# Performance work log

Hardware: AMD Instinct MI355X
Metric: run time of the kernel (lower is better)

Reference implementation:

```python
import jax, jax.numpy as jnp
import numpy as np

# dims: B batch, L residues, CS=c_s, N_EXP mHC streams, H heads, CH c_hidden,
# PQK/PV qk/v points, CZ=c_p pair channels, RANK z-factor rank, CZQ=CZ//4
B, L, CS, N_EXP, H, CH, PQK, PV, CZ, RANK = 4, 1024, 384, 4, 8, 64, 4, 8, 128, 2
CZQ = CZ // 4
SINKHORN_ITERS = 20


def quat_to_rot(q):
    q = q / jnp.sqrt((q * q).sum(-1, keepdims=True) + 1e-8)
    w, x, y, z = q[..., 0], q[..., 1], q[..., 2], q[..., 3]
    R = jnp.stack([
        1 - 2 * (y * y + z * z), 2 * (x * y - w * z), 2 * (x * z + w * y),
        2 * (x * y + w * z), 1 - 2 * (x * x + z * z), 2 * (y * z - w * x),
        2 * (x * z - w * y), 2 * (y * z + w * x), 1 - 2 * (x * x + y * y)], axis=-1)
    return R.reshape(q.shape[:-1] + (3, 3))


def layer_norm(x, g, b, eps=1e-5):
    mu = x.mean(-1, keepdims=True)
    var = ((x - mu) ** 2).mean(-1, keepdims=True)
    return (x - mu) * jax.lax.rsqrt(var + eps) * g + b


def sinkhorn(logits):
    # project onto doubly-stochastic matrices (Birkhoff polytope), fixed iters
    M = jnp.exp(logits - logits.max(axis=(-2, -1), keepdims=True))
    for _ in range(SINKHORN_ITERS):
        M = M / (M.sum(-1, keepdims=True) + 1e-8)
        M = M / (M.sum(-2, keepdims=True) + 1e-8)
    return M


def _forward(s, z_factor_1, z_factor_2, quat_t, trans, mask, b_pre, b_post, b_res,
             W_pre, W_post, W_res, alpha, Wq, Wk, Wv, Wq_pts, Wk_pts, Wv_pts,
             Wz_q, Wz_k, head_w, Wo, bo, ln1_g, ln1_b, Wt1, bt1, Wt2, bt2,
             Wt3, bt3, lnt_g, lnt_b, Wbb, bbb):
    # --- mHC: expand_input (first layer replicates stream) + dynamic mappings ---
    s_exp = jnp.broadcast_to(s[:, :, None, :], (B, L, N_EXP, CS))
    h = s_exp.reshape(B, L, N_EXP * CS)
    hn = h * jax.lax.rsqrt((h * h).mean(-1, keepdims=True) + 1e-6)
    H_pre = jax.nn.softmax(b_pre + alpha * (hn @ W_pre), -1)        # [B,L,n]
    H_post = 2.0 * jax.nn.sigmoid(b_post + alpha * (hn @ W_post))   # [B,L,n]
    H_res = sinkhorn(b_res + alpha * (hn @ W_res).reshape(B, L, N_EXP, N_EXP))
    s_c = jnp.einsum('bln,blnc->blc', H_pre, s_exp)                 # contraction

    rot = quat_to_rot(quat_t)                                       # [B,L,3,3]

    # --- Flash-IPA (dense math-equivalent reference) ---
    q = (s_c @ Wq).reshape(B, L, H, CH)
    k = (s_c @ Wk).reshape(B, L, H, CH)
    v = (s_c @ Wv).reshape(B, L, H, CH)
    qp = (s_c @ Wq_pts).reshape(B, L, H, PQK, 3)
    kp = (s_c @ Wk_pts).reshape(B, L, H, PQK, 3)
    vp = (s_c @ Wv_pts).reshape(B, L, H, PV, 3)

    def to_global(p):
        return jnp.einsum('blij,blhpj->blhpi', rot, p) + trans[:, :, None, None, :]

    qp_g, kp_g, vp_g = to_global(qp), to_global(kp), to_global(vp)

    # low-rank factorized pair bias (z = outer product of per-residue factors)
    zq = jnp.einsum('blrz,zh->blrh', z_factor_1, Wz_q)
    zk = jnp.einsum('blrz,zh->blrh', z_factor_1, Wz_k)
    bias = jnp.einsum('birh,bjrh->bhij', zq, zk)

    qk = jnp.einsum('bihc,bjhc->bhij', q, k) / np.sqrt(CH)
    qn = (qp_g ** 2).sum((-2, -1)).transpose(0, 2, 1)               # [B,H,L]
    kn = (kp_g ** 2).sum((-2, -1)).transpose(0, 2, 1)
    pdot = jnp.einsum('bihpd,bjhpd->bhij', qp_g, kp_g)
    d2 = qn[:, :, :, None] + kn[:, :, None, :] - 2.0 * pdot         # sum_p ||qp_i - kp_j||^2
    gamma = jax.nn.softplus(head_w)
    wC = np.sqrt(2.0 / (9.0 * PQK))
    wL = np.sqrt(1.0 / 3.0)
    logits = wL * (qk + bias) - (wL * wC * 0.5) * gamma[None, :, None, None] * d2
    logits = jnp.where(mask[:, None, None, :] > 0, logits, -1e9)
    a = jax.nn.softmax(logits, -1)

    o = jnp.einsum('bhij,bjhc->bihc', a, v).reshape(B, L, H * CH)
    opt_g = jnp.einsum('bhij,bjhpd->bihpd', a, vp_g)
    diff = opt_g - trans[:, :, None, None, :]
    opt_l = jnp.einsum('blij,blhpi->blhpj', rot, diff)              # R^T (x - t)
    opt_norm = jnp.sqrt((opt_l ** 2).sum(-1) + 1e-8)
    opair = jnp.einsum('bhij,bjhrc->bihrc', a, z_factor_2).reshape(B, L, H * RANK * CZQ)
    feat = jnp.concatenate([o, opt_l.reshape(B, L, H * PV * 3),
                            opt_norm.reshape(B, L, H * PV), opair], -1)
    ipa_out = feat @ Wo + bo

    # residual + (dropout=identity at eval) + LN + transition (residual MLP) + LN
    s1 = layer_norm(s_c + ipa_out, ln1_g, ln1_b)
    t1 = jax.nn.relu(s1 @ Wt1 + bt1)
    t2 = jax.nn.relu(t1 @ Wt2 + bt2)
    s_ipa = layer_norm(s1 + (t2 @ Wt3 + bt3), lnt_g, lnt_b)

    # backbone update: quaternion (1,b,c,d) + translation, composed with frame
    upd = s_ipa @ Wbb + bbb                                         # [B,L,6]
    quat_u = jnp.concatenate([jnp.ones((B, L, 1), upd.dtype), upd[..., :3]], -1)
    R_u = quat_to_rot(quat_u)
    rot_new = jnp.einsum('blij,bljk->blik', rot, R_u)
    trans_new = jnp.einsum('blij,blj->bli', rot, upd[..., 3:]) + trans

    # mHC combine: H_res @ s  +  H_post^T * s_ipa (broadcast over streams)
    s_out = jnp.einsum('blmn,blnc->blmc', H_res, s_exp) + H_post[..., None] * s_ipa[:, :, None, :]
    return s_out, rot_new, trans_new


def setup_inputs() -> dict:
    key = jax.random.key(0)
    ks = jax.random.split(key, 24)

    def nrm(k, shape, scale=1.0):
        return jax.random.normal(k, shape, jnp.float32) * scale

    FEAT = H * CH + H * PV * 4 + H * RANK * CZQ  # 512 + 256 + 512 = 1280
    return dict(
        s=nrm(ks[0], (B, L, CS)),
        z_factor_1=nrm(ks[1], (B, L, RANK, CZ)),
        z_factor_2=nrm(ks[2], (B, L, H, RANK, CZQ)),
        quat_t=nrm(ks[3], (B, L, 4)),
        trans=nrm(ks[4], (B, L, 3)),
        mask=jnp.ones((B, L), jnp.float32),
        b_pre=nrm(ks[5], (N_EXP,), 0.02),
        b_post=nrm(ks[6], (N_EXP,), 0.02),
        b_res=nrm(ks[7], (N_EXP, N_EXP), 0.02),
        W_pre=nrm(ks[8], (N_EXP * CS, N_EXP), 0.02),
        W_post=nrm(ks[9], (N_EXP * CS, N_EXP), 0.02),
        W_res=nrm(ks[10], (N_EXP * CS, N_EXP * N_EXP), 0.02),
        alpha=jnp.float32(0.01),
        Wq=nrm(ks[11], (CS, H * CH), 0.02),
        Wk=nrm(ks[12], (CS, H * CH), 0.02),
        Wv=nrm(ks[13], (CS, H * CH), 0.02),
        Wq_pts=nrm(ks[14], (CS, H * PQK * 3), 0.02),
        Wk_pts=nrm(ks[15], (CS, H * PQK * 3), 0.02),
        Wv_pts=nrm(ks[16], (CS, H * PV * 3), 0.02),
        Wz_q=nrm(ks[17], (CZ, H), 0.02),
        Wz_k=nrm(ks[18], (CZ, H), 0.02),
        head_w=jnp.zeros((H,), jnp.float32),
        Wo=nrm(ks[19], (FEAT, CS), 0.02),
        bo=jnp.zeros((CS,), jnp.float32),
        ln1_g=jnp.ones((CS,), jnp.float32),
        ln1_b=jnp.zeros((CS,), jnp.float32),
        Wt1=nrm(ks[20], (CS, CS), 0.02),
        bt1=jnp.zeros((CS,), jnp.float32),
        Wt2=nrm(ks[21], (CS, CS), 0.02),
        bt2=jnp.zeros((CS,), jnp.float32),
        Wt3=nrm(ks[22], (CS, CS), 0.02),
        bt3=jnp.zeros((CS,), jnp.float32),
        lnt_g=jnp.ones((CS,), jnp.float32),
        lnt_b=jnp.zeros((CS,), jnp.float32),
        Wbb=nrm(ks[23], (CS, 6), 0.02),
        bbb=jnp.zeros((6,), jnp.float32),
    )


def reference(s, z_factor_1, z_factor_2, quat_t, trans, mask, b_pre, b_post, b_res,
              W_pre, W_post, W_res, alpha, Wq, Wk, Wv, Wq_pts, Wk_pts, Wv_pts,
              Wz_q, Wz_k, head_w, Wo, bo, ln1_g, ln1_b, Wt1, bt1, Wt2, bt2,
              Wt3, bt3, lnt_g, lnt_b, Wbb, bbb):
    return _forward(s, z_factor_1, z_factor_2, quat_t, trans, mask, b_pre, b_post,
                    b_res, W_pre, W_post, W_res, alpha, Wq, Wk, Wv, Wq_pts, Wk_pts,
                    Wv_pts, Wz_q, Wz_k, head_w, Wo, bo, ln1_g, ln1_b, Wt1, bt1,
                    Wt2, bt2, Wt3, bt3, lnt_g, lnt_b, Wbb, bbb)
```

## Files before the change

### kernel.cpp

```cpp
#include <hip/hip_runtime.h>
#include <hip/hip_bf16.h>

typedef __hip_bfloat16 bf16;
typedef float f4v __attribute__((ext_vector_type(4)));
typedef short s8v __attribute__((ext_vector_type(8)));

#define CSD    384
#define LL     1024
#define NH     8
#define BL     4096
#define NPROJ  1920
#define QDP    96
#define VDP    160
#define FEATD  1280

#define OFF_S      0
#define OFF_Z1     1572864
#define OFF_Z2     2621440
#define OFF_QUAT   4718592
#define OFF_TRANS  4734976
#define OFF_MASK   4747264
#define OFF_BPOST  4751360
#define OFF_BRES   4751376
#define OFF_WPOST  4751392
#define OFF_WRES   4757536
#define OFF_ALPHA  4782112
#define OFF_WQ     4782128
#define OFF_WK     4978736
#define OFF_WV     5175344
#define OFF_WQP    5371952
#define OFF_WKP    5408816
#define OFF_WVP    5445680
#define OFF_WZQ    5519408
#define OFF_WZK    5520432
#define OFF_HEADW  5521456
#define OFF_WO     5521472
#define OFF_BO     6012992
#define OFF_LN1G   6013376
#define OFF_LN1B   6013760
#define OFF_WT1    6014144
#define OFF_BT1    6161600
#define OFF_WT2    6161984
#define OFF_BT2    6309440
#define OFF_WT3    6309824
#define OFF_BT3    6457280
#define OFF_LNTG   6457664
#define OFF_LNTB   6458048
#define OFF_WBB    6458432
#define OFF_BBB    6460736
#define IN_END     6460752

#define WS_FLAG    6460752
#define WS_WPOSTR  6460768
#define WS_WRESR   6462304
#define WS_HPOST   6468448
#define WS_ROWSUM  6484832
#define WS_ROTB    6501216
#define WS_WCATT   6538080
#define WS_PROJ    7275360
#define WS_QB      15139680
#define WS_KB      16712544
#define WS_VT      18285408
#define WS_WOT     20906848
#define WS_WT1T    21152608
#define WS_WT2T    21226336
#define WS_WT3T    21300064
#define WS_VROW    21373792

#define OUT_ROT 6291456
#define OUT_TR  6328320

#define NSEG 34

struct P36 { const void* p[36]; };

__device__ __forceinline__ float b2f(bf16 x) { return __bfloat162float(x); }

__device__ __forceinline__ short f2bs(float x) {
  unsigned u = __float_as_uint(x);
  u += 0x7FFFu + ((u >> 16) & 1u);
  return (short)(u >> 16);
}

__device__ __forceinline__ int packbf(float lo, float hi) {
  return (int)(unsigned short)f2bs(lo) | ((int)f2bs(hi) << 16);
}

__device__ __forceinline__ float wredf(float v) {
#pragma unroll
  for (int o = 1; o < 64; o <<= 1) v += __shfl_xor(v, o, 64);
  return v;
}

__global__ void detect_k(const unsigned int* __restrict__ mask_raw, int* __restrict__ flag) {
  if (threadIdx.x == 0 && blockIdx.x == 0) flag[0] = (mask_raw[0] == 0x3F803F80u) ? 1 : 0;
}

__global__ __launch_bounds__(256) void cvtall_k(P36 ptrs, float* __restrict__ dst, const int* __restrict__ flagp) {
  const int i = blockIdx.x * 256 + threadIdx.x;
  if (i >= IN_END) return;
  const int flag = flagp[0];
  const int seg_src_t[NSEG] = {0,1,2,3,4,5,7,8,10,11,12,13,14,15,16,17,18,19,20,21,22,23,24,25,26,27,28,29,30,31,32,33,34,35};
  const int seg_dst_t[NSEG] = {OFF_S,OFF_Z1,OFF_Z2,OFF_QUAT,OFF_TRANS,OFF_MASK,OFF_BPOST,OFF_BRES,OFF_WPOST,OFF_WRES,
                               OFF_ALPHA,OFF_WQ,OFF_WK,OFF_WV,OFF_WQP,OFF_WKP,OFF_WVP,OFF_WZQ,OFF_WZK,OFF_HEADW,
                               OFF_WO,OFF_BO,OFF_LN1G,OFF_LN1B,OFF_WT1,OFF_BT1,OFF_WT2,OFF_BT2,OFF_WT3,OFF_BT3,
                               OFF_LNTG,OFF_LNTB,OFF_WBB,OFF_BBB};
  const int seg_cnt_t[NSEG] = {1572864,1048576,2097152,16384,12288,4096,4,16,6144,24576,
                               1,196608,196608,196608,36864,36864,73728,1024,1024,8,
                               491520,384,384,384,147456,384,147456,384,147456,384,
                               384,384,2304,6};
  int off = i, cnt = seg_cnt_t[0];
  const void* sp = ptrs.p[0];
#pragma unroll
  for (int k = 1; k < NSEG; k++) {
    if (i >= seg_dst_t[k]) { off = i - seg_dst_t[k]; cnt = seg_cnt_t[k]; sp = ptrs.p[seg_src_t[k]]; }
  }
  float v = 0.f;
  if (off < cnt) {
    v = flag ? b2f(((const bf16*)sp)[off]) : ((const float*)sp)[off];
  }
  dst[i] = v;
}

__global__ __launch_bounds__(256) void wcatT_k(const float* __restrict__ Wq, const float* __restrict__ Wk,
                                               const float* __restrict__ Wv, const float* __restrict__ Wqp,
                                               const float* __restrict__ Wkp, const float* __restrict__ Wvp,
                                               short* __restrict__ WcatT) {
  int i = blockIdx.x * 256 + threadIdx.x;
  if (i >= CSD * NPROJ) return;
  int k = i / NPROJ, c = i % NPROJ;
  float v;
  if (c < 512)       v = Wq[k * 512 + c];
  else if (c < 1024) v = Wk[k * 512 + c - 512];
  else if (c < 1536) v = Wv[k * 512 + c - 1024];
  else if (c < 1632) v = Wqp[k * 96 + c - 1536];
  else if (c < 1728) v = Wkp[k * 96 + c - 1632];
  else               v = Wvp[k * 192 + c - 1728];
  WcatT[c * CSD + k] = f2bs(v);
}

__global__ __launch_bounds__(256) void wT_k(const float* __restrict__ W, short* __restrict__ Wt, int K, int N) {
  int i = blockIdx.x * 256 + threadIdx.x;
  if (i >= K * N) return;
  int k = i / N, n = i % N;
  Wt[(size_t)n * K + k] = f2bs(W[i]);
}

__global__ __launch_bounds__(256) void wreduce_k(const float* __restrict__ Wpost, const float* __restrict__ Wres,
                                                 float* __restrict__ WpostR, float* __restrict__ WresR) {
  int i = blockIdx.x * 256 + threadIdx.x;
  if (i < CSD * 4) {
    int c = i >> 2, n = i & 3;
    float s = 0.f;
#pragma unroll
    for (int blk = 0; blk < 4; blk++) s += Wpost[(blk * CSD + c) * 4 + n];
    WpostR[i] = s;
  }
  if (i < CSD * 16) {
    int c = i >> 4, n = i & 15;
    float s = 0.f;
#pragma unroll
    for (int blk = 0; blk < 4; blk++) s += Wres[(blk * CSD + c) * 16 + n];
    WresR[i] = s;
  }
}

__global__ __launch_bounds__(64) void mhc_k(const float* __restrict__ sF, const float* __restrict__ quat,
                                            const float* __restrict__ bpost, const float* __restrict__ bres,
                                            const float* __restrict__ alpha_p, const float* __restrict__ WpostR,
                                            const float* __restrict__ WresR, float* __restrict__ hpost,
                                            float* __restrict__ rowsum, float* __restrict__ rotb) {
  const int bl = blockIdx.x, t = threadIdx.x;
  const float* sr = sF + (size_t)bl * CSD;
  float ssq = 0.f, dp[4] = {0.f, 0.f, 0.f, 0.f}, dr[16];
#pragma unroll
  for (int n = 0; n < 16; n++) dr[n] = 0.f;
#pragma unroll
  for (int e = 0; e < 6; e++) {
    const int c = t + e * 64;
    const float sv = sr[c];
    ssq = fmaf(sv, sv, ssq);
#pragma unroll
    for (int n = 0; n < 4; n++) dp[n] = fmaf(sv, WpostR[c * 4 + n], dp[n]);
#pragma unroll
    for (int n = 0; n < 16; n++) dr[n] = fmaf(sv, WresR[c * 16 + n], dr[n]);
  }
  ssq = wredf(ssq);
#pragma unroll
  for (int n = 0; n < 4; n++) dp[n] = wredf(dp[n]);
#pragma unroll
  for (int n = 0; n < 16; n++) dr[n] = wredf(dr[n]);
  const float alpha = alpha_p[0];
  const float invn = rsqrtf(ssq * (1.f / 384.f) + 1e-6f);
  if (t == 0) {
#pragma unroll
    for (int n = 0; n < 4; n++) {
      const float x = bpost[n] + alpha * invn * dp[n];
      hpost[bl * 4 + n] = 2.f / (1.f + __expf(-x));
    }
    float M[16];
    float mx = -1e30f;
#pragma unroll
    for (int k = 0; k < 16; k++) { M[k] = bres[k] + alpha * invn * dr[k]; mx = fmaxf(mx, M[k]); }
#pragma unroll
    for (int k = 0; k < 16; k++) M[k] = __expf(M[k] - mx);
    for (int it = 0; it < 20; it++) {
#pragma unroll
      for (int r = 0; r < 4; r++) {
        const float s4 = M[r * 4] + M[r * 4 + 1] + M[r * 4 + 2] + M[r * 4 + 3];
        const float iv = 1.f / (s4 + 1e-8f);
        M[r * 4] *= iv; M[r * 4 + 1] *= iv; M[r * 4 + 2] *= iv; M[r * 4 + 3] *= iv;
      }
#pragma unroll
      for (int c2 = 0; c2 < 4; c2++) {
        const float s4 = M[c2] + M[4 + c2] + M[8 + c2] + M[12 + c2];
        const float iv = 1.f / (s4 + 1e-8f);
        M[c2] *= iv; M[4 + c2] *= iv; M[8 + c2] *= iv; M[12 + c2] *= iv;
      }
    }
#pragma unroll
    for (int r = 0; r < 4; r++)
      rowsum[bl * 4 + r] = M[r * 4] + M[r * 4 + 1] + M[r * 4 + 2] + M[r * 4 + 3];
  }
  if (t == 1) {
    float w = quat[bl * 4 + 0], x = quat[bl * 4 + 1];
    float y = quat[bl * 4 + 2], z = quat[bl * 4 + 3];
    const float iq = rsqrtf(w * w + x * x + y * y + z * z + 1e-8f);
    w *= iq; x *= iq; y *= iq; z *= iq;
    float* R = rotb + (size_t)bl * 9;
    R[0] = 1.f - 2.f * (y * y + z * z); R[1] = 2.f * (x * y - w * z); R[2] = 2.f * (x * z + w * y);
    R[3] = 2.f * (x * y + w * z); R[4] = 1.f - 2.f * (x * x + z * z); R[5] = 2.f * (y * z - w * x);
    R[6] = 2.f * (x * z - w * y); R[7] = 2.f * (y * z + w * x); R[8] = 1.f - 2.f * (x * x + y * y);
  }
}

__global__ __launch_bounds__(256) void gemm_mfma_k(const float* __restrict__ A, const short* __restrict__ Bt,
                                                   const float* __restrict__ bias, float* __restrict__ C,
                                                   int M, int N, int K, int relu) {
  __shared__ __align__(16) short As[128 * 40];
  __shared__ __align__(16) short Bs[128 * 40];
  const int tid = threadIdx.x;
  const int wid = tid >> 6, lane = tid & 63;
  const int c15 = lane & 15, q = lane >> 4;
  const int bm = blockIdx.y, bn = blockIdx.x;
  const int m_wave = (wid & 1) * 64, n_wave = (wid >> 1) * 64;
  const float* Ab = A + (size_t)(bm * 128) * K;
  const short* Bb = Bt + (size_t)(bn * 128) * K;

  f4v acc[4][4];
#pragma unroll
  for (int mi = 0; mi < 4; mi++)
#pragma unroll
    for (int ni = 0; ni < 4; ni++) acc[mi][ni] = (f4v){0.f, 0.f, 0.f, 0.f};

  for (int k0 = 0; k0 < K; k0 += 32) {
    __syncthreads();
#pragma unroll
    for (int e = 0; e < 4; e++) {
      const int slot = tid + e * 256;
      const int m = slot >> 3, k4 = (slot & 7) * 4;
      const float4 a = *(const float4*)(Ab + (size_t)m * K + k0 + k4);
      short pk[4] = {f2bs(a.x), f2bs(a.y), f2bs(a.z), f2bs(a.w)};
      *(int2*)&As[m * 40 + k4] = *(const int2*)pk;
    }
#pragma unroll
    for (int e = 0; e < 2; e++) {
      const int slot = tid + e * 256;
      const int n = slot >> 2, k8 = (slot & 3) * 8;
      *(int4*)&Bs[n * 40 + k8] = *(const int4*)(Bb + (size_t)n * K + k0 + k8);
    }
    __syncthreads();
    s8v Af[4], Bf[4];
#pragma unroll
    for (int mi = 0; mi < 4; mi++) Af[mi] = *(const s8v*)&As[(m_wave + mi * 16 + c15) * 40 + q * 8];
#pragma unroll
    for (int ni = 0; ni < 4; ni++) Bf[ni] = *(const s8v*)&Bs[(n_wave + ni * 16 + c15) * 40 + q * 8];
#pragma unroll
    for (int mi = 0; mi < 4; mi++)
#pragma unroll
      for (int ni = 0; ni < 4; ni++)
        acc[mi][ni] = __builtin_amdgcn_mfma_f32_16x16x32_bf16(Af[mi], Bf[ni], acc[mi][ni], 0, 0, 0);
  }
#pragma unroll
  for (int mi = 0; mi < 4; mi++) {
#pragma unroll
    for (int r = 0; r < 4; r++) {
      const int row = bm * 128 + m_wave + mi * 16 + q * 4 + r;
      float* Cr = C + (size_t)row * N + bn * 128 + n_wave;
#pragma unroll
      for (int ni = 0; ni < 4; ni++) {
        const int col = bn * 128 + n_wave + ni * 16 + c15;
        float v = acc[mi][ni][r];
        if (bias != nullptr) v += bias[col];
        if (relu) v = fmaxf(v, 0.f);
        Cr[ni * 16 + c15] = v;
      }
    }
  }
}

__global__ __launch_bounds__(256) void assemble_k(const float* __restrict__ proj, const float* __restrict__ rotb,
                                                  const float* __restrict__ trans, const float* __restrict__ z1,
                                                  const float* __restrict__ z2, const float* __restrict__ Wzq,
                                                  const float* __restrict__ Wzk, const float* __restrict__ headw,
                                                  int* __restrict__ Qo4, int* __restrict__ Ko4,
                                                  int* __restrict__ Vr4) {
  const int idx = blockIdx.x * 256 + threadIdx.x;
  const int h = idx & 7, bl = idx >> 3;
  const float* pr = proj + (size_t)bl * NPROJ;
  const float* R = rotb + (size_t)bl * 9;
  const float txx = trans[bl * 3 + 0], tyy = trans[bl * 3 + 1], tzz = trans[bl * 3 + 2];
  float gamma;
  { const float w = headw[h]; gamma = (w > 20.f) ? w : log1pf(__expf(w)); }
  const float wL = 0.57735026918962576f;
  const float wC = 0.23570226039551584f;
  const float ch = wL * wC * 0.5f * gamma;
  const float qscale = wL * 0.125f;

  float zq0 = 0.f, zq1 = 0.f, zk0 = 0.f, zk1 = 0.f;
  const float* z1r = z1 + (size_t)bl * 256;
  for (int zz = 0; zz < 128; zz++) {
    const float wq = Wzq[zz * 8 + h], wk = Wzk[zz * 8 + h];
    const float a0 = z1r[zz], a1 = z1r[128 + zz];
    zq0 = fmaf(a0, wq, zq0); zq1 = fmaf(a1, wq, zq1);
    zk0 = fmaf(a0, wk, zk0); zk1 = fmaf(a1, wk, zk1);
  }
  const int b = bl >> 10, l = bl & 1023;
  const size_t row = (size_t)(b * NH + h) * LL + l;
  int* Qo = Qo4 + row * 48;
  int* Ko = Ko4 + row * 48;
  int* Vo = Vr4 + row * 80;
#pragma unroll
  for (int g = 0; g < 8; g++) {
    int4 qi, ki, vi;
#pragma unroll
    for (int t2 = 0; t2 < 4; t2++) {
      const int c = g * 8 + t2 * 2;
      ((int*)&qi)[t2] = packbf(pr[h * 64 + c] * qscale, pr[h * 64 + c + 1] * qscale);
      ((int*)&ki)[t2] = packbf(pr[512 + h * 64 + c], pr[512 + h * 64 + c + 1]);
      ((int*)&vi)[t2] = packbf(pr[1024 + h * 64 + c], pr[1024 + h * 64 + c + 1]);
    }
    ((int4*)Qo)[g] = qi; ((int4*)Ko)[g] = ki; ((int4*)Vo)[g] = vi;
  }
  float qt16[16], kt16[16];
  qt16[0] = wL * zq0; qt16[1] = wL * zq1;
  kt16[0] = zk0; kt16[1] = zk1;
  float qn = 0.f, kn = 0.f;
#pragma unroll
  for (int p = 0; p < 4; p++) {
    const float* pl = pr + 1536 + h * 12 + p * 3;
    float gx = R[0] * pl[0] + R[1] * pl[1] + R[2] * pl[2] + txx;
    float gy = R[3] * pl[0] + R[4] * pl[1] + R[5] * pl[2] + tyy;
    float gz = R[6] * pl[0] + R[7] * pl[1] + R[8] * pl[2] + tzz;
    qn += gx * gx + gy * gy + gz * gz;
    qt16[2 + p * 3 + 0] = 2.f * ch * gx; qt16[2 + p * 3 + 1] = 2.f * ch * gy; qt16[2 + p * 3 + 2] = 2.f * ch * gz;
    const float* pk = pr + 1632 + h * 12 + p * 3;
    gx = R[0] * pk[0] + R[1] * pk[1] + R[2] * pk[2] + txx;
    gy = R[3] * pk[0] + R[4] * pk[1] + R[5] * pk[2] + tyy;
    gz = R[6] * pk[0] + R[7] * pk[1] + R[8] * pk[2] + tzz;
    kn += gx * gx + gy * gy + gz * gz;
    kt16[2 + p * 3 + 0] = gx; kt16[2 + p * 3 + 1] = gy; kt16[2 + p * 3 + 2] = gz;
  }
  qt16[14] = -ch * qn; qt16[15] = 1.f;
  kt16[14] = 1.f;      kt16[15] = -ch * kn;
#pragma unroll
  for (int g = 0; g < 2; g++) {
    int4 qi, ki;
#pragma unroll
    for (int t2 = 0; t2 < 4; t2++) {
      const int c = g * 8 + t2 * 2;
      ((int*)&qi)[t2] = packbf(qt16[c], qt16[c + 1]);
      ((int*)&ki)[t2] = packbf(kt16[c], kt16[c + 1]);
    }
    ((int4*)Qo)[8 + g] = qi; ((int4*)Ko)[8 + g] = ki;
  }
  int4 z4; z4.x = 0; z4.y = 0; z4.z = 0; z4.w = 0;
  ((int4*)Qo)[10] = z4; ((int4*)Qo)[11] = z4;
  ((int4*)Ko)[10] = z4; ((int4*)Ko)[11] = z4;
  float vt24[24];
#pragma unroll
  for (int p = 0; p < 8; p++) {
    const float* pv = pr + 1728 + h * 24 + p * 3;
    vt24[p * 3 + 0] = R[0] * pv[0] + R[1] * pv[1] + R[2] * pv[2] + txx;
    vt24[p * 3 + 1] = R[3] * pv[0] + R[4] * pv[1] + R[5] * pv[2] + tyy;
    vt24[p * 3 + 2] = R[6] * pv[0] + R[7] * pv[1] + R[8] * pv[2] + tzz;
  }
#pragma unroll
  for (int g = 0; g < 3; g++) {
    int4 vi;
#pragma unroll
    for (int t2 = 0; t2 < 4; t2++) {
      const int c = g * 8 + t2 * 2;
      ((int*)&vi)[t2] = packbf(vt24[c], vt24[c + 1]);
    }
    ((int4*)Vo)[8 + g] = vi;
  }
  const float* z2r = z2 + ((size_t)bl * NH + h) * 64;
#pragma unroll
  for (int g = 0; g < 8; g++) {
    int4 vi;
#pragma unroll
    for (int t2 = 0; t2 < 4; t2++) {
      const int c = g * 8 + t2 * 2;
      ((int*)&vi)[t2] = packbf(z2r[c], z2r[c + 1]);
    }
    ((int4*)Vo)[11 + g] = vi;
  }
  ((int4*)Vo)[19] = z4;
}

__global__ __launch_bounds__(256) void vtrans_k(const short* __restrict__ Vrow, short* __restrict__ Vtb) {
  __shared__ __align__(16) short T[64 * 168];
  const int tid = threadIdx.x;
  const int bh = blockIdx.y;
  const int l0 = blockIdx.x * 64;
  const short* src = Vrow + (size_t)bh * LL * VDP + (size_t)l0 * VDP;
  for (int u = tid; u < 1280; u += 256) {
    const int ll = u / 20, j = u % 20;
    *(int4*)&T[ll * 168 + j * 8] = *(const int4*)(src + (size_t)ll * VDP + j * 8);
  }
  __syncthreads();
  short* dst = Vtb + (size_t)bh * VDP * LL + l0;
  for (int u = tid; u < 1280; u += 256) {
    const int c = u >> 3, seg = u & 7;
    short tmp[8];
#pragma unroll
    for (int e = 0; e < 8; e++) tmp[e] = T[(seg * 8 + e) * 168 + c];
    *(int4*)(dst + (size_t)c * LL + seg * 8) = *(const int4*)tmp;
  }
}

__global__ __launch_bounds__(512, 4) void attn_k(const short* __restrict__ Qb, const short* __restrict__ Kb,
                                                 const short* __restrict__ Vtb, const float* __restrict__ maskF,
                                                 float* __restrict__ Oext) {
  __shared__ __align__(16) short smem[24704];
  short* Ks = smem;
  short* Vs = smem + 6656;
  short* Ps = smem + 19456;
  float* Msl = (float*)(smem + 24576);
  const int tid = threadIdx.x;
  const int wid = tid >> 6, lane = tid & 63;
  const int c15 = lane & 15, q = lane >> 4;
  const int blk = blockIdx.x;
  const int bh = blk & 31, qt = blk >> 5;
  const int b = bh >> 3, h = bh & 7;
  const int half = wid >> 2, mw = wid & 3;
  const int i0 = qt * 64 + mw * 16;

  s8v Qa[3];
  const short* Qrow = Qb + ((size_t)bh * LL + i0 + c15) * QDP;
#pragma unroll
  for (int kc = 0; kc < 3; kc++) Qa[kc] = *(const s8v*)(Qrow + kc * 32 + q * 8);

  f4v Of[10];
#pragma unroll
  for (int vt = 0; vt < 10; vt++) Of[vt] = (f4v){0.f, 0.f, 0.f, 0.f};
  float mold[4] = {-1e30f, -1e30f, -1e30f, -1e30f};
  float lsum[4] = {0.f, 0.f, 0.f, 0.f};

  const short* Kbase = Kb + (size_t)bh * LL * QDP;
  const short* Vbase = Vtb + (size_t)bh * VDP * LL;
  short* Ksl = Ks + half * 3328;
  short* Vsl = Vs + half * 6400;
  short* Pl = Ps + wid * 640;
  const float* Msw = Msl + half * 32;

  for (int jt = 0; jt < 16; jt++) {
    const int j0 = jt * 32;
    __syncthreads();
    for (int u = tid; u < 768; u += 512) {
      const int hs = u / 384, v2 = u - hs * 384;
      const int rr = v2 / 12, cc = v2 % 12;
      *(int4*)&Ks[hs * 3328 + rr * 104 + cc * 8] =
          *(const int4*)(Kbase + (size_t)(hs * 512 + j0 + rr) * QDP + cc * 8);
    }
    for (int u = tid; u < 1280; u += 512) {
      const int hs = u / 640, v2 = u - hs * 640;
      const int cc = v2 >> 2, part = v2 & 3;
      *(int4*)&Vs[hs * 6400 + cc * 40 + part * 8] =
          *(const int4*)(Vbase + (size_t)cc * LL + hs * 512 + j0 + part * 8);
    }
    if (tid < 64) Msl[tid] = maskF[b * LL + (tid >> 5) * 512 + j0 + (tid & 31)];
    __syncthreads();

    f4v Sf0 = (f4v){0.f, 0.f, 0.f, 0.f}, Sf1 = (f4v){0.f, 0.f, 0.f, 0.f};
#pragma unroll
    for (int kc = 0; kc < 3; kc++) {
      const s8v K0 = *(const s8v*)&Ksl[c15 * 104 + kc * 32 + q * 8];
      const s8v K1 = *(const s8v*)&Ksl[(16 + c15) * 104 + kc * 32 + q * 8];
      Sf0 = __builtin_amdgcn_mfma_f32_16x16x32_bf16(Qa[kc], K0, Sf0, 0, 0, 0);
      Sf1 = __builtin_amdgcn_mfma_f32_16x16x32_bf16(Qa[kc], K1, Sf1, 0, 0, 0);
    }
    const float mv0 = Msw[c15], mv1 = Msw[16 + c15];
    float lg0[4], lg1[4], tm[4], p0[4], p1[4];
#pragma unroll
    for (int r = 0; r < 4; r++) {
      lg0[r] = (mv0 > 0.f) ? Sf0[r] : -1e9f;
      lg1[r] = (mv1 > 0.f) ? Sf1[r] : -1e9f;
      tm[r] = fmaxf(lg0[r], lg1[r]);
    }
#pragma unroll
    for (int r = 0; r < 4; r++) {
      tm[r] = fmaxf(tm[r], __shfl_xor(tm[r], 1, 64));
      tm[r] = fmaxf(tm[r], __shfl_xor(tm[r], 2, 64));
      tm[r] = fmaxf(tm[r], __shfl_xor(tm[r], 4, 64));
      tm[r] = fmaxf(tm[r], __shfl_xor(tm[r], 8, 64));
    }
    const bool need = (tm[0] > mold[0]) | (tm[1] > mold[1]) | (tm[2] > mold[2]) | (tm[3] > mold[3]);
    if (__any(need)) {
      float al[4];
#pragma unroll
      for (int r = 0; r < 4; r++) {
        const float mn = fmaxf(mold[r], tm[r]);
        al[r] = __expf(mold[r] - mn);
        mold[r] = mn;
        p0[r] = __expf(lg0[r] - mn);
        p1[r] = __expf(lg1[r] - mn);
        lsum[r] = lsum[r] * al[r] + p0[r] + p1[r];
      }
#pragma unroll
      for (int vt = 0; vt < 10; vt++) {
#pragma unroll
        for (int r = 0; r < 4; r++) Of[vt][r] *= al[r];
      }
    } else {
#pragma unroll
      for (int r = 0; r < 4; r++) {
        p0[r] = __expf(lg0[r] - mold[r]);
        p1[r] = __expf(lg1[r] - mold[r]);
        lsum[r] += p0[r] + p1[r];
      }
    }
#pragma unroll
    for (int r = 0; r < 4; r++) {
      Pl[(q * 4 + r) * 40 + c15] = f2bs(p0[r]);
      Pl[(q * 4 + r) * 40 + 16 + c15] = f2bs(p1[r]);
    }
    const s8v Pa = *(const s8v*)&Pl[c15 * 40 + q * 8];
#pragma unroll
    for (int vt = 0; vt < 10; vt++) {
      const s8v Vf = *(const s8v*)&Vsl[(vt * 16 + c15) * 40 + q * 8];
      Of[vt] = __builtin_amdgcn_mfma_f32_16x16x32_bf16(Pa, Vf, Of[vt], 0, 0, 0);
    }
  }
#pragma unroll
  for (int r = 0; r < 4; r++) {
    lsum[r] += __shfl_xor(lsum[r], 1, 64);
    lsum[r] += __shfl_xor(lsum[r], 2, 64);
    lsum[r] += __shfl_xor(lsum[r], 4, 64);
    lsum[r] += __shfl_xor(lsum[r], 8, 64);
  }
  float* Obuf = (float*)smem;
  float* Mbuf = (float*)(smem + 20480);
  float* Lbuf = Mbuf + 64;
  __syncthreads();
  if (half == 1) {
#pragma unroll
    for (int r = 0; r < 4; r++) {
      const int rowi = mw * 16 + q * 4 + r;
#pragma unroll
      for (int vt = 0; vt < 10; vt++) Obuf[rowi * 160 + vt * 16 + c15] = Of[vt][r];
      if (c15 == 0) { Mbuf[rowi] = mold[r]; Lbuf[rowi] = lsum[r]; }
    }
  }
  __syncthreads();
  if (half == 0) {
#pragma unroll
    for (int r = 0; r < 4; r++) {
      const int rowi = mw * 16 + q * 4 + r;
      const float m2 = Mbuf[rowi], l2 = Lbuf[rowi];
      const float mx = fmaxf(mold[r], m2);
      const float a1 = __expf(mold[r] - mx), a2 = __expf(m2 - mx);
      const float inv = 1.f / (lsum[r] * a1 + l2 * a2);
      const int i = i0 + q * 4 + r;
      float* Or = Oext + ((size_t)(b * LL + i) * NH + h) * VDP;
#pragma unroll
      for (int vt = 0; vt < 10; vt++)
        Or[vt * 16 + c15] = (Of[vt][r] * a1 + Obuf[rowi * 160 + vt * 16 + c15] * a2) * inv;
    }
  }
}

__global__ __launch_bounds__(256) void feat_k(const float* __restrict__ Oext, const float* __restrict__ rotb,
                                              const float* __restrict__ trans, float* __restrict__ feat) {
  const int idx = blockIdx.x * 256 + threadIdx.x;
  const int h = idx & 7, bl = idx >> 3;
  const float* O = Oext + (size_t)(bl * 8 + h) * VDP;
  float* f = feat + (size_t)bl * FEATD;
  for (int c = 0; c < 64; c++) f[h * 64 + c] = O[c];
  const float* R = rotb + (size_t)bl * 9;
  const float txx = trans[bl * 3 + 0], tyy = trans[bl * 3 + 1], tzz = trans[bl * 3 + 2];
#pragma unroll
  for (int p = 0; p < 8; p++) {
    const float dx = O[64 + p * 3 + 0] - txx;
    const float dy = O[64 + p * 3 + 1] - tyy;
    const float dz = O[64 + p * 3 + 2] - tzz;
    const float lx = R[0] * dx + R[3] * dy + R[6] * dz;
    const float ly = R[1] * dx + R[4] * dy + R[7] * dz;
    const float lz = R[2] * dx + R[5] * dy + R[8] * dz;
    f[512 + h * 24 + p * 3 + 0] = lx;
    f[512 + h * 24 + p * 3 + 1] = ly;
    f[512 + h * 24 + p * 3 + 2] = lz;
    f[704 + h * 8 + p] = sqrtf(lx * lx + ly * ly + lz * lz + 1e-8f);
  }
  for (int c = 0; c < 64; c++) f[768 + h * 64 + c] = O[88 + c];
}

__global__ __launch_bounds__(64) void ln_k(const float* __restrict__ x, const float* __restrict__ resid,
                                           const float* __restrict__ g, const float* __restrict__ bta,
                                           float* __restrict__ out) {
  const int row = blockIdx.x, t = threadIdx.x;
  const float* xr = x + (size_t)row * CSD;
  const float* rr = resid + (size_t)row * CSD;
  float v[6];
  float s = 0.f;
#pragma unroll
  for (int e = 0; e < 6; e++) {
    const int c = t + e * 64;
    v[e] = xr[c] + rr[c];
    s += v[e];
  }
  s = wredf(s);
  const float mu = s * (1.f / 384.f);
  float var = 0.f;
#pragma unroll
  for (int e = 0; e < 6; e++) { const float d = v[e] - mu; var = fmaf(d, d, var); }
  var = wredf(var) * (1.f / 384.f);
  const float inv = rsqrtf(var + 1e-5f);
#pragma unroll
  for (int e = 0; e < 6; e++) {
    const int c = t + e * 64;
    out[(size_t)row * CSD + c] = (v[e] - mu) * inv * g[c] + bta[c];
  }
}

__global__ __launch_bounds__(64) void final_k(const float* __restrict__ sF, const float* __restrict__ sipa,
                                              const float* __restrict__ rotb, const float* __restrict__ trans,
                                              const float* __restrict__ hpost, const float* __restrict__ rowsum,
                                              const float* __restrict__ Wbb, const float* __restrict__ bbb,
                                              const int* __restrict__ flagp, void* __restrict__ outv) {
  const int bl = blockIdx.x, t = threadIdx.x;
  const int flag = flagp[0];
  bf16* outb = (bf16*)outv;
  float* outf = (float*)outv;
  const float* si = sipa + (size_t)bl * CSD;
  float d6[6] = {0.f, 0.f, 0.f, 0.f, 0.f, 0.f};
#pragma unroll
  for (int e = 0; e < 6; e++) {
    const int c = t + e * 64;
    const float v = si[c];
#pragma unroll
    for (int u = 0; u < 6; u++) d6[u] = fmaf(v, Wbb[c * 6 + u], d6[u]);
  }
#pragma unroll
  for (int u = 0; u < 6; u++) d6[u] = wredf(d6[u]);
  float upd[6];
#pragma unroll
  for (int u = 0; u < 6; u++) upd[u] = d6[u] + bbb[u];
  const float* R = rotb + (size_t)bl * 9;
  if (t == 0) {
    float w = 1.f, x = upd[0], y = upd[1], z = upd[2];
    const float iq = rsqrtf(w * w + x * x + y * y + z * z + 1e-8f);
    w *= iq; x *= iq; y *= iq; z *= iq;
    const float Ru[9] = {1.f - 2.f * (y * y + z * z), 2.f * (x * y - w * z), 2.f * (x * z + w * y),
                         2.f * (x * y + w * z), 1.f - 2.f * (x * x + z * z), 2.f * (y * z - w * x),
                         2.f * (x * z - w * y), 2.f * (y * z + w * x), 1.f - 2.f * (x * x + y * y)};
#pragma unroll
    for (int i = 0; i < 3; i++)
#pragma unroll
      for (int j = 0; j < 3; j++) {
        const float rv = R[i * 3 + 0] * Ru[0 + j] + R[i * 3 + 1] * Ru[3 + j] + R[i * 3 + 2] * Ru[6 + j];
        const size_t o = OUT_ROT + (size_t)bl * 9 + i * 3 + j;
        if (flag) outb[o] = __float2bfloat16(rv); else outf[o] = rv;
      }
#pragma unroll
    for (int i = 0; i < 3; i++) {
      const float tv = R[i * 3 + 0] * upd[3] + R[i * 3 + 1] * upd[4] + R[i * 3 + 2] * upd[5] + trans[bl * 3 + i];
      const size_t o = OUT_TR + (size_t)bl * 3 + i;
      if (flag) outb[o] = __float2bfloat16(tv); else outf[o] = tv;
    }
  }
  const float hp0 = hpost[bl * 4 + 0], hp1 = hpost[bl * 4 + 1], hp2 = hpost[bl * 4 + 2], hp3 = hpost[bl * 4 + 3];
  const float rs0 = rowsum[bl * 4 + 0], rs1 = rowsum[bl * 4 + 1], rs2 = rowsum[bl * 4 + 2], rs3 = rowsum[bl * 4 + 3];
  const float* sr = sF + (size_t)bl * CSD;
#pragma unroll
  for (int e = 0; e < 6; e++) {
    const int c = t + e * 64;
    const float sv = sr[c], sp = si[c];
    const size_t base = (size_t)bl * 4 * CSD + c;
    const float o0 = rs0 * sv + hp0 * sp;
    const float o1 = rs1 * sv + hp1 * sp;
    const float o2 = rs2 * sv + hp2 * sp;
    const float o3 = rs3 * sv + hp3 * sp;
    if (flag) {
      outb[base + 0 * CSD] = __float2bfloat16(o0);
      outb[base + 1 * CSD] = __float2bfloat16(o1);
      outb[base + 2 * CSD] = __float2bfloat16(o2);
      outb[base + 3 * CSD] = __float2bfloat16(o3);
    } else {
      outf[base + 0 * CSD] = o0;
      outf[base + 1 * CSD] = o1;
      outf[base + 2 * CSD] = o2;
      outf[base + 3 * CSD] = o3;
    }
  }
}

extern "C" void kernel_launch(void* const* d_in, const int* in_sizes, int n_in,
                              void* d_out, int out_size, void* d_ws, size_t ws_size,
                              hipStream_t stream) {
  float* ws = (float*)d_ws;
  int* flag = (int*)(ws + WS_FLAG);

  P36 ptrs;
  for (int i = 0; i < 36; i++) ptrs.p[i] = d_in[i];

  float* sF     = ws + OFF_S;
  float* WpostR = ws + WS_WPOSTR;
  float* WresR  = ws + WS_WRESR;
  float* hpost  = ws + WS_HPOST;
  float* rowsum = ws + WS_ROWSUM;
  float* rotb   = ws + WS_ROTB;
  short* WcatT  = (short*)(ws + WS_WCATT);
  short* WoT    = (short*)(ws + WS_WOT);
  short* Wt1T   = (short*)(ws + WS_WT1T);
  short* Wt2T   = (short*)(ws + WS_WT2T);
  short* Wt3T   = (short*)(ws + WS_WT3T);
  float* proj   = ws + WS_PROJ;
  short* Qb     = (short*)(ws + WS_QB);
  short* Kb     = (short*)(ws + WS_KB);
  short* Vtb    = (short*)(ws + WS_VT);
  short* Vrow   = (short*)(ws + WS_VROW);
  float* Oext   = ws + WS_PROJ;
  float* featb  = ws + WS_QB;
  float* x1s1   = ws + WS_PROJ;
  float* t1b    = ws + WS_QB;
  float* t2b    = ws + WS_KB;
  float* x3     = ws + WS_PROJ + 1572864;
  float* sipa   = ws + WS_KB;

  detect_k<<<1, 64, 0, stream>>>((const unsigned int*)d_in[5], flag);
  cvtall_k<<<(IN_END + 255) / 256, 256, 0, stream>>>(ptrs, ws, flag);
  wcatT_k<<<2880, 256, 0, stream>>>(ws + OFF_WQ, ws + OFF_WK, ws + OFF_WV,
                                    ws + OFF_WQP, ws + OFF_WKP, ws + OFF_WVP, WcatT);
  wT_k<<<1920, 256, 0, stream>>>(ws + OFF_WO, WoT, FEATD, CSD);
  wT_k<<<576, 256, 0, stream>>>(ws + OFF_WT1, Wt1T, CSD, CSD);
  wT_k<<<576, 256, 0, stream>>>(ws + OFF_WT2, Wt2T, CSD, CSD);
  wT_k<<<576, 256, 0, stream>>>(ws + OFF_WT3, Wt3T, CSD, CSD);
  wreduce_k<<<24, 256, 0, stream>>>(ws + OFF_WPOST, ws + OFF_WRES, WpostR, WresR);
  mhc_k<<<BL, 64, 0, stream>>>(sF, ws + OFF_QUAT, ws + OFF_BPOST, ws + OFF_BRES, ws + OFF_ALPHA,
                               WpostR, WresR, hpost, rowsum, rotb);
  gemm_mfma_k<<<dim3(15, 32), 256, 0, stream>>>(sF, WcatT, nullptr, proj, BL, NPROJ, CSD, 0);
  assemble_k<<<128, 256, 0, stream>>>(proj, rotb, ws + OFF_TRANS, ws + OFF_Z1, ws + OFF_Z2,
                                      ws + OFF_WZQ, ws + OFF_WZK, ws + OFF_HEADW,
                                      (int*)Qb, (int*)Kb, (int*)Vrow);
  vtrans_k<<<dim3(16, 32), 256, 0, stream>>>(Vrow, Vtb);
  attn_k<<<512, 512, 0, stream>>>(Qb, Kb, Vtb, ws + OFF_MASK, Oext);
  feat_k<<<128, 256, 0, stream>>>(Oext, rotb, ws + OFF_TRANS, featb);
  gemm_mfma_k<<<dim3(3, 32), 256, 0, stream>>>(featb, WoT, ws + OFF_BO, x1s1, BL, CSD, FEATD, 0);
  ln_k<<<BL, 64, 0, stream>>>(x1s1, sF, ws + OFF_LN1G, ws + OFF_LN1B, x1s1);
  gemm_mfma_k<<<dim3(3, 32), 256, 0, stream>>>(x1s1, Wt1T, ws + OFF_BT1, t1b, BL, CSD, CSD, 1);
  gemm_mfma_k<<<dim3(3, 32), 256, 0, stream>>>(t1b, Wt2T, ws + OFF_BT2, t2b, BL, CSD, CSD, 1);
  gemm_mfma_k<<<dim3(3, 32), 256, 0, stream>>>(t2b, Wt3T, ws + OFF_BT3, x3, BL, CSD, CSD, 0);
  ln_k<<<BL, 64, 0, stream>>>(x3, x1s1, ws + OFF_LNTG, ws + OFF_LNTB, sipa);
  final_k<<<BL, 64, 0, stream>>>(sF, sipa, rotb, ws + OFF_TRANS, hpost, rowsum,
                                 ws + OFF_WBB, ws + OFF_BBB, flag, d_out);
}
```

Measured before the change: 542.4 us.

## Fuse prep, assemble/vtrans, and LN/final kernels; stop converting z inputs

Several changes land together. The weight transposes move into one tiled kernel that stages through shared memory. The z factors are read raw inside assemble instead of being converted to fp32 first. Assemble now writes V transposed directly, which removes vtrans, and both assemble and feat are parallelised as one 64-thread block per residue. The final layer norm is fused into the final output kernel. The aim is fewer launches, less global traffic and better occupancy, at the cost of uncoalesced strided bf16 stores for transposed V.

```diff
diff --git a/kernel.cpp b/kernel.cpp
--- a/kernel.cpp
+++ b/kernel.cpp
@@ -15,62 +15,59 @@
 #define FEATD  1280
 
 #define OFF_S      0
-#define OFF_Z1     1572864
-#define OFF_Z2     2621440
-#define OFF_QUAT   4718592
-#define OFF_TRANS  4734976
-#define OFF_MASK   4747264
-#define OFF_BPOST  4751360
-#define OFF_BRES   4751376
-#define OFF_WPOST  4751392
-#define OFF_WRES   4757536
-#define OFF_ALPHA  4782112
-#define OFF_WQ     4782128
-#define OFF_WK     4978736
-#define OFF_WV     5175344
-#define OFF_WQP    5371952
-#define OFF_WKP    5408816
-#define OFF_WVP    5445680
-#define OFF_WZQ    5519408
-#define OFF_WZK    5520432
-#define OFF_HEADW  5521456
-#define OFF_WO     5521472
-#define OFF_BO     6012992
-#define OFF_LN1G   6013376
-#define OFF_LN1B   6013760
-#define OFF_WT1    6014144
-#define OFF_BT1    6161600
-#define OFF_WT2    6161984
-#define OFF_BT2    6309440
-#define OFF_WT3    6309824
-#define OFF_BT3    6457280
-#define OFF_LNTG   6457664
-#define OFF_LNTB   6458048
-#define OFF_WBB    6458432
-#define OFF_BBB    6460736
-#define IN_END     6460752
-
-#define WS_FLAG    6460752
-#define WS_WPOSTR  6460768
-#define WS_WRESR   6462304
-#define WS_HPOST   6468448
-#define WS_ROWSUM  6484832
-#define WS_ROTB    6501216
-#define WS_WCATT   6538080
-#define WS_PROJ    7275360
-#define WS_QB      15139680
-#define WS_KB      16712544
-#define WS_VT      18285408
-#define WS_WOT     20906848
-#define WS_WT1T    21152608
-#define WS_WT2T    21226336
-#define WS_WT3T    21300064
-#define WS_VROW    21373792
+#define OFF_QUAT   1572864
+#define OFF_TRANS  1589248
+#define OFF_MASK   1601536
+#define OFF_BPOST  1605632
+#define OFF_BRES   1605648
+#define OFF_WPOST  1605664
+#define OFF_WRES   1611808
+#define OFF_ALPHA  1636384
+#define OFF_WQ     1636400
+#define OFF_WK     1833008
+#define OFF_WV     2029616
+#define OFF_WQP    2226224
+#define OFF_WKP    2263088
+#define OFF_WVP    2299952
+#define OFF_WZQ    2373680
+#define OFF_WZK    2374704
+#define OFF_HEADW  2375728
+#define OFF_WO     2375744
+#define OFF_BO     2867264
+#define OFF_LN1G   2867648
+#define OFF_LN1B   2868032
+#define OFF_WT1    2868416
+#define OFF_BT1    3015872
+#define OFF_WT2    3016256
+#define OFF_BT2    3163712
+#define OFF_WT3    3164096
+#define OFF_BT3    3311552
+#define OFF_LNTG   3311936
+#define OFF_LNTB   3312320
+#define OFF_WBB    3312704
+#define OFF_BBB    3315008
+#define IN_END     3315024
+
+#define WS_FLAG    3315024
+#define WS_WPOSTR  3315040
+#define WS_WRESR   3316576
+#define WS_HPOST   3322720
+#define WS_ROWSUM  3339104
+#define WS_ROTB    3355488
+#define WS_WCATT   3392352
+#define WS_WOT     3760992
+#define WS_WT1T    4006752
+#define WS_WT2T    4080480
+#define WS_WT3T    4154208
+#define WS_PROJ    4227936
+#define WS_QB      12092256
+#define WS_KB      13665120
+#define WS_VT      15237984
 
 #define OUT_ROT 6291456
 #define OUT_TR  6328320
 
-#define NSEG 34
+#define NSEG 32
 
 struct P36 { const void* p[36]; };
 
@@ -86,6 +83,10 @@
   return (int)(unsigned short)f2bs(lo) | ((int)f2bs(hi) << 16);
 }
 
+__device__ __forceinline__ float ldraw(const void* p, size_t i, int flag) {
+  return flag ? b2f(((const bf16*)p)[i]) : ((const float*)p)[i];
+}
+
 __device__ __forceinline__ float wredf(float v) {
 #pragma unroll
   for (int o = 1; o < 64; o <<= 1) v += __shfl_xor(v, o, 64);
@@ -100,13 +101,13 @@
   const int i = blockIdx.x * 256 + threadIdx.x;
   if (i >= IN_END) return;
   const int flag = flagp[0];
-  const int seg_src_t[NSEG] = {0,1,2,3,4,5,7,8,10,11,12,13,14,15,16,17,18,19,20,21,22,23,24,25,26,27,28,29,30,31,32,33,34,35};
-  const int seg_dst_t[NSEG] = {OFF_S,OFF_Z1,OFF_Z2,OFF_QUAT,OFF_TRANS,OFF_MASK,OFF_BPOST,OFF_BRES,OFF_WPOST,OFF_WRES,
-                               OFF_ALPHA,OFF_WQ,OFF_WK,OFF_WV,OFF_WQP,OFF_WKP,OFF_WVP,OFF_WZQ,OFF_WZK,OFF_HEADW,
+  const int seg_src_t[NSEG] = {0,3,4,5,7,8,10,11,12,13,14,15,16,17,18,19,20,21,22,23,24,25,26,27,28,29,30,31,32,33,34,35};
+  const int seg_dst_t[NSEG] = {OFF_S,OFF_QUAT,OFF_TRANS,OFF_MASK,OFF_BPOST,OFF_BRES,OFF_WPOST,OFF_WRES,OFF_ALPHA,
+                               OFF_WQ,OFF_WK,OFF_WV,OFF_WQP,OFF_WKP,OFF_WVP,OFF_WZQ,OFF_WZK,OFF_HEADW,
                                OFF_WO,OFF_BO,OFF_LN1G,OFF_LN1B,OFF_WT1,OFF_BT1,OFF_WT2,OFF_BT2,OFF_WT3,OFF_BT3,
                                OFF_LNTG,OFF_LNTB,OFF_WBB,OFF_BBB};
-  const int seg_cnt_t[NSEG] = {1572864,1048576,2097152,16384,12288,4096,4,16,6144,24576,
-                               1,196608,196608,196608,36864,36864,73728,1024,1024,8,
+  const int seg_cnt_t[NSEG] = {1572864,16384,12288,4096,4,16,6144,24576,1,
+                               196608,196608,196608,36864,36864,73728,1024,1024,8,
                                491520,384,384,384,147456,384,147456,384,147456,384,
                                384,384,2304,6};
   int off = i, cnt = seg_cnt_t[0];
@@ -116,34 +117,42 @@
     if (i >= seg_dst_t[k]) { off = i - seg_dst_t[k]; cnt = seg_cnt_t[k]; sp = ptrs.p[seg_src_t[k]]; }
   }
   float v = 0.f;
-  if (off < cnt) {
-    v = flag ? b2f(((const bf16*)sp)[off]) : ((const float*)sp)[off];
-  }
+  if (off < cnt) v = flag ? b2f(((const bf16*)sp)[off]) : ((const float*)sp)[off];
   dst[i] = v;
 }
 
-__global__ __launch_bounds__(256) void wcatT_k(const float* __restrict__ Wq, const float* __restrict__ Wk,
-                                               const float* __restrict__ Wv, const float* __restrict__ Wqp,
-                                               const float* __restrict__ Wkp, const float* __restrict__ Wvp,
-                                               short* __restrict__ WcatT) {
-  int i = blockIdx.x * 256 + threadIdx.x;
-  if (i >= CSD * NPROJ) return;
-  int k = i / NPROJ, c = i % NPROJ;
-  float v;
-  if (c < 512)       v = Wq[k * 512 + c];
-  else if (c < 1024) v = Wk[k * 512 + c - 512];
-  else if (c < 1536) v = Wv[k * 512 + c - 1024];
-  else if (c < 1632) v = Wqp[k * 96 + c - 1536];
-  else if (c < 1728) v = Wkp[k * 96 + c - 1632];
-  else               v = Wvp[k * 192 + c - 1728];
-  WcatT[c * CSD + k] = f2bs(v);
-}
-
-__global__ __launch_bounds__(256) void wT_k(const float* __restrict__ W, short* __restrict__ Wt, int K, int N) {
-  int i = blockIdx.x * 256 + threadIdx.x;
-  if (i >= K * N) return;
-  int k = i / N, n = i % N;
-  Wt[(size_t)n * K + k] = f2bs(W[i]);
+__global__ __launch_bounds__(256) void wprep_k(const float* __restrict__ ws, short* __restrict__ wsS) {
+  const int jobs_src[10] = {OFF_WQ, OFF_WK, OFF_WV, OFF_WQP, OFF_WKP, OFF_WVP, OFF_WO, OFF_WT1, OFF_WT2, OFF_WT3};
+  const int jobs_dst[10] = {WS_WCATT*2, WS_WCATT*2 + 512*384, WS_WCATT*2 + 1024*384, WS_WCATT*2 + 1536*384,
+                            WS_WCATT*2 + 1632*384, WS_WCATT*2 + 1728*384, WS_WOT*2, WS_WT1T*2, WS_WT2T*2, WS_WT3T*2};
+  const int jobs_K[10] = {384,384,384,384,384,384,1280,384,384,384};
+  const int jobs_N[10] = {512,512,512,96,96,192,384,384,384,384};
+  const int jobs_t0[10] = {0,192,384,576,612,648,720,1200,1344,1488};
+  const int t = blockIdx.x;
+  int j = 0;
+#pragma unroll
+  for (int k = 1; k < 10; k++) if (t >= jobs_t0[k]) j = k;
+  const int tl = t - jobs_t0[j];
+  const int K = jobs_K[j], N = jobs_N[j];
+  const int ntn = N >> 5;
+  const int kt = tl / ntn, nt = tl - kt * ntn;
+  const int k0 = kt * 32, n0 = nt * 32;
+  const float* src = ws + jobs_src[j];
+  short* dst = wsS + jobs_dst[j];
+  __shared__ float T[32][36];
+  {
+    const int r = threadIdx.x >> 3, cq = (threadIdx.x & 7) * 4;
+    const float4 a = *(const float4*)(src + (size_t)(k0 + r) * N + n0 + cq);
+    T[r][cq] = a.x; T[r][cq + 1] = a.y; T[r][cq + 2] = a.z; T[r][cq + 3] = a.w;
+  }
+  __syncthreads();
+  {
+    const int n = threadIdx.x >> 3, kq = (threadIdx.x & 7) * 4;
+    short pk4[4];
+#pragma unroll
+    for (int e = 0; e < 4; e++) pk4[e] = f2bs(T[kq + e][n]);
+    *(int2*)(dst + (size_t)(n0 + n) * K + k0 + kq) = *(const int2*)pk4;
+  }
 }
 
 __global__ __launch_bounds__(256) void wreduce_k(const float* __restrict__ Wpost, const float* __restrict__ Wres,
@@ -299,14 +308,16 @@
   }
 }
 
-__global__ __launch_bounds__(256) void assemble_k(const float* __restrict__ proj, const float* __restrict__ rotb,
-                                                  const float* __restrict__ trans, const float* __restrict__ z1,
-                                                  const float* __restrict__ z2, const float* __restrict__ Wzq,
-                                                  const float* __restrict__ Wzk, const float* __restrict__ headw,
-                                                  int* __restrict__ Qo4, int* __restrict__ Ko4,
-                                                  int* __restrict__ Vr4) {
-  const int idx = blockIdx.x * 256 + threadIdx.x;
-  const int h = idx & 7, bl = idx >> 3;
+__global__ __launch_bounds__(64) void assemble_k(const float* __restrict__ proj, const float* __restrict__ rotb,
+                                                 const float* __restrict__ trans, const void* __restrict__ z1raw,
+                                                 const void* __restrict__ z2raw, const float* __restrict__ Wzq,
+                                                 const float* __restrict__ Wzk, const float* __restrict__ headw,
+                                                 const int* __restrict__ flagp, short* __restrict__ Qb,
+                                                 short* __restrict__ Kb, short* __restrict__ Vtb) {
+  __shared__ float qt[8][16], kt[8][16];
+  const int bl = blockIdx.x, lane = threadIdx.x;
+  const int h = lane >> 3, sub = lane & 7;
+  const int flag = flagp[0];
   const float* pr = proj + (size_t)bl * NPROJ;
   const float* R = rotb + (size_t)bl * 9;
   const float txx = trans[bl * 3 + 0], tyy = trans[bl * 3 + 1], tzz = trans[bl * 3 + 2];
@@ -318,122 +329,112 @@
   const float qscale = wL * 0.125f;
 
   float zq0 = 0.f, zq1 = 0.f, zk0 = 0.f, zk1 = 0.f;
-  const float* z1r = z1 + (size_t)bl * 256;
-  for (int zz = 0; zz < 128; zz++) {
+  const size_t zbase = (size_t)bl * 256;
+  for (int zz = sub; zz < 128; zz += 8) {
+    const float a0 = ldraw(z1raw, zbase + zz, flag);
+    const float a1 = ldraw(z1raw, zbase + 128 + zz, flag);
     const float wq = Wzq[zz * 8 + h], wk = Wzk[zz * 8 + h];
-    const float a0 = z1r[zz], a1 = z1r[128 + zz];
     zq0 = fmaf(a0, wq, zq0); zq1 = fmaf(a1, wq, zq1);
     zk0 = fmaf(a0, wk, zk0); zk1 = fmaf(a1, wk, zk1);
   }
+#pragma unroll
+  for (int o = 1; o < 8; o <<= 1) {
+    zq0 += __shfl_xor(zq0, o, 64); zq1 += __shfl_xor(zq1, o, 64);
+    zk0 += __shfl_xor(zk0, o, 64); zk1 += __shfl_xor(zk1, o, 64);
+  }
+
   const int b = bl >> 10, l = bl & 1023;
-  const size_t row = (size_t)(b * NH + h) * LL + l;
-  int* Qo = Qo4 + row * 48;
-  int* Ko = Ko4 + row * 48;
-  int* Vo = Vr4 + row * 80;
-#pragma unroll
-  for (int g = 0; g < 8; g++) {
-    int4 qi, ki, vi;
-#pragma unroll
-    for (int t2 = 0; t2 < 4; t2++) {
-      const int c = g * 8 + t2 * 2;
-      ((int*)&qi)[t2] = packbf(pr[h * 64 + c] * qscale, pr[h * 64 + c + 1] * qscale);
-      ((int*)&ki)[t2] = packbf(pr[512 + h * 64 + c], pr[512 + h * 64 + c + 1]);
-      ((int*)&vi)[t2] = packbf(pr[1024 + h * 64 + c], pr[1024 + h * 64 + c + 1]);
-    }
-    ((int4*)Qo)[g] = qi; ((int4*)Ko)[g] = ki; ((int4*)Vo)[g] = vi;
-  }
-  float qt16[16], kt16[16];
-  qt16[0] = wL * zq0; qt16[1] = wL * zq1;
-  kt16[0] = zk0; kt16[1] = zk1;
-  float qn = 0.f, kn = 0.f;
-#pragma unroll
-  for (int p = 0; p < 4; p++) {
-    const float* pl = pr + 1536 + h * 12 + p * 3;
-    float gx = R[0] * pl[0] + R[1] * pl[1] + R[2] * pl[2] + txx;
-    float gy = R[3] * pl[0] + R[4] * pl[1] + R[5] * pl[2] + tyy;
-    float gz = R[6] * pl[0] + R[7] * pl[1] + R[8] * pl[2] + tzz;
-    qn += gx * gx + gy * gy + gz * gz;
-    qt16[2 + p * 3 + 0] = 2.f * ch * gx; qt16[2 + p * 3 + 1] = 2.f * ch * gy; qt16[2 + p * 3 + 2] = 2.f * ch * gz;
-    const float* pk = pr + 1632 + h * 12 + p * 3;
-    gx = R[0] * pk[0] + R[1] * pk[1] + R[2] * pk[2] + txx;
-    gy = R[3] * pk[0] + R[4] * pk[1] + R[5] * pk[2] + tyy;
-    gz = R[6] * pk[0] + R[7] * pk[1] + R[8] * pk[2] + tzz;
-    kn += gx * gx + gy * gy + gz * gz;
-    kt16[2 + p * 3 + 0] = gx; kt16[2 + p * 3 + 1] = gy; kt16[2 + p * 3 + 2] = gz;
-  }
-  qt16[14] = -ch * qn; qt16[15] = 1.f;
-  kt16[14] = 1.f;      kt16[15] = -ch * kn;
-#pragma unroll
-  for (int g = 0; g < 2; g++) {
-    int4 qi, ki;
-#pragma unroll
-    for (int t2 = 0; t2 < 4; t2++) {
-      const int c = g * 8 + t2 * 2;
-      ((int*)&qi)[t2] = packbf(qt16[c], qt16[c + 1]);
-      ((int*)&ki)[t2] = packbf(kt16[c], kt16[c + 1]);
-    }
-    ((int4*)Qo)[8 + g] = qi; ((int4*)Ko)[8 + g] = ki;
-  }
-  int4 z4; z4.x = 0; z4.y = 0; z4.z = 0; z4.w = 0;
-  ((int4*)Qo)[10] = z4; ((int4*)Qo)[11] = z4;
-  ((int4*)Ko)[10] = z4; ((int4*)Ko)[11] = z4;
-  float vt24[24];
-#pragma unroll
-  for (int p = 0; p < 8; p++) {
-    const float* pv = pr + 1728 + h * 24 + p * 3;
-    vt24[p * 3 + 0] = R[0] * pv[0] + R[1] * pv[1] + R[2] * pv[2] + txx;
-    vt24[p * 3 + 1] = R[3] * pv[0] + R[4] * pv[1] + R[5] * pv[2] + tyy;
-    vt24[p * 3 + 2] = R[6] * pv[0] + R[7] * pv[1] + R[8] * pv[2] + tzz;
-  }
-#pragma unroll
-  for (int g = 0; g < 3; g++) {
-    int4 vi;
-#pragma unroll
-    for (int t2 = 0; t2 < 4; t2++) {
-      const int c = g * 8 + t2 * 2;
-      ((int*)&vi)[t2] = packbf(vt24[c], vt24[c + 1]);
-    }
-    ((int4*)Vo)[8 + g] = vi;
-  }
-  const float* z2r = z2 + ((size_t)bl * NH + h) * 64;
-#pragma unroll
-  for (int g = 0; g < 8; g++) {
-    int4 vi;
-#pragma unroll
-    for (int t2 = 0; t2 < 4; t2++) {
-      const int c = g * 8 + t2 * 2;
-      ((int*)&vi)[t2] = packbf(z2r[c], z2r[c + 1]);
-    }
-    ((int4*)Vo)[11 + g] = vi;
-  }
-  ((int4*)Vo)[19] = z4;
-}
-
-__global__ __launch_bounds__(256) void vtrans_k(const short* __restrict__ Vrow, short* __restrict__ Vtb) {
-  __shared__ __align__(16) short T[64 * 168];
-  const int tid = threadIdx.x;
-  const int bh = blockIdx.y;
-  const int l0 = blockIdx.x * 64;
-  const short* src = Vrow + (size_t)bh * LL * VDP + (size_t)l0 * VDP;
-  for (int u = tid; u < 1280; u += 256) {
-    const int ll = u / 20, j = u % 20;
-    *(int4*)&T[ll * 168 + j * 8] = *(const int4*)(src + (size_t)ll * VDP + j * 8);
-  }
-  __syncthreads();
-  short* dst = Vtb + (size_t)bh * VDP * LL + l0;
-  for (int u = tid; u < 1280; u += 256) {
-    const int c = u >> 3, seg = u & 7;
-    short tmp[8];
-#pragma unroll
-    for (int e = 0; e < 8; e++) tmp[e] = T[(seg * 8 + e) * 168 + c];
-    *(int4*)(dst + (size_t)c * LL + seg * 8) = *(const int4*)tmp;
+  const int bh = b * NH + h;
+  const size_t row = (size_t)bh * LL + l;
+  short* Q = Qb + row * QDP;
+  short* Kx = Kb + row * QDP;
+
+  {
+    const float* ps = pr + h * 64 + sub * 8;
+    const float4 a0 = ((const float4*)ps)[0], a1 = ((const float4*)ps)[1];
+    int4 qi;
+    qi.x = packbf(a0.x * qscale, a0.y * qscale); qi.y = packbf(a0.z * qscale, a0.w * qscale);
+    qi.z = packbf(a1.x * qscale, a1.y * qscale); qi.w = packbf(a1.z * qscale, a1.w * qscale);
+    ((int4*)Q)[sub] = qi;
+    const float* pk = pr + 512 + h * 64 + sub * 8;
+    const float4 b0 = ((const float4*)pk)[0], b1 = ((const float4*)pk)[1];
+    int4 ki;
+    ki.x = packbf(b0.x, b0.y); ki.y = packbf(b0.z, b0.w);
+    ki.z = packbf(b1.x, b1.y); ki.w = packbf(b1.z, b1.w);
+    ((int4*)Kx)[sub] = ki;
+    const float* pv = pr + 1024 + h * 64 + sub * 8;
+#pragma unroll
+    for (int e = 0; e < 8; e++)
+      Vtb[((size_t)bh * VDP + sub * 8 + e) * LL + l] = f2bs(pv[e]);
+  }
+
+  {
+    const float* pp = pr + ((sub < 4) ? 1536 : 1632) + h * 12 + (sub & 3) * 3;
+    const float gx = R[0] * pp[0] + R[1] * pp[1] + R[2] * pp[2] + txx;
+    const float gy = R[3] * pp[0] + R[4] * pp[1] + R[5] * pp[2] + tyy;
+    const float gz = R[6] * pp[0] + R[7] * pp[1] + R[8] * pp[2] + tzz;
+    float nrm = gx * gx + gy * gy + gz * gz;
+    nrm += __shfl_xor(nrm, 1, 64);
+    nrm += __shfl_xor(nrm, 2, 64);
+    const float other = __shfl_xor(nrm, 4, 64);
+    const float qn = (sub < 4) ? nrm : other;
+    const float kn = (sub < 4) ? other : nrm;
+    if (sub < 4) {
+      qt[h][2 + sub * 3 + 0] = 2.f * ch * gx;
+      qt[h][2 + sub * 3 + 1] = 2.f * ch * gy;
+      qt[h][2 + sub * 3 + 2] = 2.f * ch * gz;
+    } else {
+      kt[h][2 + (sub - 4) * 3 + 0] = gx;
+      kt[h][2 + (sub - 4) * 3 + 1] = gy;
+      kt[h][2 + (sub - 4) * 3 + 2] = gz;
+    }
+    if (sub == 0) {
+      qt[h][0] = wL * zq0; qt[h][1] = wL * zq1; qt[h][14] = -ch * qn; qt[h][15] = 1.f;
+      kt[h][0] = zk0;      kt[h][1] = zk1;      kt[h][14] = 1.f;      kt[h][15] = -ch * kn;
+    }
+  }
+  {
+    int4 z4; z4.x = 0; z4.y = 0; z4.z = 0; z4.w = 0;
+    if (sub < 2) {
+      const float* s4 = &qt[h][sub * 8];
+      int4 qi;
+      qi.x = packbf(s4[0], s4[1]); qi.y = packbf(s4[2], s4[3]);
+      qi.z = packbf(s4[4], s4[5]); qi.w = packbf(s4[6], s4[7]);
+      ((int4*)Q)[8 + sub] = qi;
+    } else if (sub < 4) {
+      const float* s4 = &kt[h][(sub - 2) * 8];
+      int4 ki;
+      ki.x = packbf(s4[0], s4[1]); ki.y = packbf(s4[2], s4[3]);
+      ki.z = packbf(s4[4], s4[5]); ki.w = packbf(s4[6], s4[7]);
+      ((int4*)Kx)[8 + sub - 2] = ki;
+    } else if (sub == 4) ((int4*)Q)[10] = z4;
+    else if (sub == 5) ((int4*)Q)[11] = z4;
+    else if (sub == 6) ((int4*)Kx)[10] = z4;
+    else ((int4*)Kx)[11] = z4;
+  }
+  {
+    const float* pv3 = pr + 1728 + h * 24 + sub * 3;
+    const float gx = R[0] * pv3[0] + R[1] * pv3[1] + R[2] * pv3[2] + txx;
+    const float gy = R[3] * pv3[0] + R[4] * pv3[1] + R[5] * pv3[2] + tyy;
+    const float gz = R[6] * pv3[0] + R[7] * pv3[1] + R[8] * pv3[2] + tzz;
+    const int c = 64 + sub * 3;
+    Vtb[((size_t)bh * VDP + c + 0) * LL + l] = f2bs(gx);
+    Vtb[((size_t)bh * VDP + c + 1) * LL + l] = f2bs(gy);
+    Vtb[((size_t)bh * VDP + c + 2) * LL + l] = f2bs(gz);
+  }
+  {
+    const size_t z2base = ((size_t)bl * NH + h) * 64 + sub * 8;
+#pragma unroll
+    for (int e = 0; e < 8; e++)
+      Vtb[((size_t)bh * VDP + 88 + sub * 8 + e) * LL + l] = f2bs(ldraw(z2raw, z2base + e, flag));
+    Vtb[((size_t)bh * VDP + 152 + sub) * LL + l] = 0;
   }
 }
 
 __global__ __launch_bounds__(512, 4) void attn_k(const short* __restrict__ Qb, const short* __restrict__ Kb,
                                                  const short* __restrict__ Vtb, const float* __restrict__ maskF,
                                                  float* __restrict__ Oext) {
-  __shared__ __align__(16) short smem[24704];
+  __shared__ __align__(16) short smem[26624];
   short* Ks = smem;
   short* Vs = smem + 6656;
   short* Ps = smem + 19456;
@@ -442,10 +443,13 @@
   const int wid = tid >> 6, lane = tid & 63;
   const int c15 = lane & 15, q = lane >> 4;
   const int blk = blockIdx.x;
-  const int bh = blk & 31, qt = blk >> 5;
+  const int bh = blk & 31, qt2 = blk >> 5;
   const int b = bh >> 3, h = bh & 7;
   const int half = wid >> 2, mw = wid & 3;
-  const int i0 = qt * 64 + mw * 16;
+  const int i0 = qt2 * 64 + mw * 16;
+
+  const short* Kbase = Kb + (size_t)bh * LL * QDP;
+  const short* Vbase = Vtb + (size_t)bh * VDP * LL;
 
   s8v Qa[3];
   const short* Qrow = Qb + ((size_t)bh * LL + i0 + c15) * QDP;
@@ -458,30 +462,47 @@
   float mold[4] = {-1e30f, -1e30f, -1e30f, -1e30f};
   float lsum[4] = {0.f, 0.f, 0.f, 0.f};
 
-  const short* Kbase = Kb + (size_t)bh * LL * QDP;
-  const short* Vbase = Vtb + (size_t)bh * VDP * LL;
+  Msl[tid] = maskF[b * LL + tid];
+  Msl[tid + 512] = maskF[b * LL + tid + 512];
+
+  const int khs0 = tid / 384;
+  const int kv0 = tid - khs0 * 384;
+  const int krr0 = kv0 / 12, kcc0 = kv0 - krr0 * 12;
+  int khs1 = 0, krr1 = 0, kcc1 = 0;
+  if (tid < 256) { const int u = tid + 512; khs1 = u / 384; const int v2 = u - khs1 * 384; krr1 = v2 / 12; kcc1 = v2 - krr1 * 12; }
+  const int vhs0 = tid / 640; const int vv0 = tid - vhs0 * 640; const int vcc0 = vv0 >> 2, vp0 = vv0 & 3;
+  const int vhs1 = (tid + 512) / 640; const int vv1 = (tid + 512) - vhs1 * 640; const int vcc1 = vv1 >> 2, vp1 = vv1 & 3;
+  int vhs2 = 0, vcc2 = 0, vp2 = 0;
+  if (tid < 256) { const int u = tid + 1024; vhs2 = u / 640; const int v2 = u - vhs2 * 640; vcc2 = v2 >> 2; vp2 = v2 & 3; }
+
+  int4 kr0, kr1, vr0, vr1, vr2;
+  kr0 = *(const int4*)(Kbase + (size_t)(khs0 * 512 + krr0) * QDP + kcc0 * 8);
+  if (tid < 256) kr1 = *(const int4*)(Kbase + (size_t)(khs1 * 512 + krr1) * QDP + kcc1 * 8);
+  vr0 = *(const int4*)(Vbase + (size_t)vcc0 * LL + vhs0 * 512 + vp0 * 8);
+  vr1 = *(const int4*)(Vbase + (size_t)vcc1 * LL + vhs1 * 512 + vp1 * 8);
+  if (tid < 256) vr2 = *(const int4*)(Vbase + (size_t)vcc2 * LL + vhs2 * 512 + vp2 * 8);
+
   short* Ksl = Ks + half * 3328;
   short* Vsl = Vs + half * 6400;
   short* Pl = Ps + wid * 640;
-  const float* Msw = Msl + half * 32;
 
   for (int jt = 0; jt < 16; jt++) {
     const int j0 = jt * 32;
     __syncthreads();
-    for (int u = tid; u < 768; u += 512) {
-      const int hs = u / 384, v2 = u - hs * 384;
-      const int rr = v2 / 12, cc = v2 % 12;
-      *(int4*)&Ks[hs * 3328 + rr * 104 + cc * 8] =
-          *(const int4*)(Kbase + (size_t)(hs * 512 + j0 + rr) * QDP + cc * 8);
-    }
-    for (int u = tid; u < 1280; u += 512) {
-      const int hs = u / 640, v2 = u - hs * 640;
-      const int cc = v2 >> 2, part = v2 & 3;
-      *(int4*)&Vs[hs * 6400 + cc * 40 + part * 8] =
-          *(const int4*)(Vbase + (size_t)cc * LL + hs * 512 + j0 + part * 8);
-    }
-    if (tid < 64) Msl[tid] = maskF[b * LL + (tid >> 5) * 512 + j0 + (tid & 31)];
+    *(int4*)&Ks[khs0 * 3328 + krr0 * 104 + kcc0 * 8] = kr0;
+    if (tid < 256) *(int4*)&Ks[khs1 * 3328 + krr1 * 104 + kcc1 * 8] = kr1;
+    *(int4*)&Vs[vhs0 * 6400 + vcc0 * 40 + vp0 * 8] = vr0;
+    *(int4*)&Vs[vhs1 * 6400 + vcc1 * 40 + vp1 * 8] = vr1;
+    if (tid < 256) *(int4*)&Vs[vhs2 * 6400 + vcc2 * 40 + vp2 * 8] = vr2;
     __syncthreads();
+    if (jt < 15) {
+      const int j0n = j0 + 32;
+      kr0 = *(const int4*)(Kbase + (size_t)(khs0 * 512 + j0n + krr0) * QDP + kcc0 * 8);
+      if (tid < 256) kr1 = *(const int4*)(Kbase + (size_t)(khs1 * 512 + j0n + krr1) * QDP + kcc1 * 8);
+      vr0 = *(const int4*)(Vbase + (size_t)vcc0 * LL + vhs0 * 512 + j0n + vp0 * 8);
+      vr1 = *(const int4*)(Vbase + (size_t)vcc1 * LL + vhs1 * 512 + j0n + vp1 * 8);
+      if (tid < 256) vr2 = *(const int4*)(Vbase + (size_t)vcc2 * LL + vhs2 * 512 + j0n + vp2 * 8);
+    }
 
     f4v Sf0 = (f4v){0.f, 0.f, 0.f, 0.f}, Sf1 = (f4v){0.f, 0.f, 0.f, 0.f};
 #pragma unroll
@@ -491,7 +512,8 @@
       Sf0 = __builtin_amdgcn_mfma_f32_16x16x32_bf16(Qa[kc], K0, Sf0, 0, 0, 0);
       Sf1 = __builtin_amdgcn_mfma_f32_16x16x32_bf16(Qa[kc], K1, Sf1, 0, 0, 0);
     }
-    const float mv0 = Msw[c15], mv1 = Msw[16 + c15];
+    const float mv0 = Msl[half * 512 + j0 + c15];
+    const float mv1 = Msl[half * 512 + j0 + 16 + c15];
     float lg0[4], lg1[4], tm[4], p0[4], p1[4];
 #pragma unroll
     for (int r = 0; r < 4; r++) {
@@ -581,29 +603,34 @@
   }
 }
 
-__global__ __launch_bounds__(256) void feat_k(const float* __restrict__ Oext, const float* __restrict__ rotb,
-                                              const float* __restrict__ trans, float* __restrict__ feat) {
-  const int idx = blockIdx.x * 256 + threadIdx.x;
-  const int h = idx & 7, bl = idx >> 3;
-  const float* O = Oext + (size_t)(bl * 8 + h) * VDP;
+__global__ __launch_bounds__(64) void feat_k(const float* __restrict__ Oext, const float* __restrict__ rotb,
+                                             const float* __restrict__ trans, float* __restrict__ feat) {
+  const int bl = blockIdx.x, lane = threadIdx.x;
+  const int h = lane >> 3, sub = lane & 7;
+  const float* O = Oext + ((size_t)bl * 8 + h) * VDP;
   float* f = feat + (size_t)bl * FEATD;
-  for (int c = 0; c < 64; c++) f[h * 64 + c] = O[c];
+  {
+    const float4 a0 = ((const float4*)(O + sub * 8))[0], a1 = ((const float4*)(O + sub * 8))[1];
+    ((float4*)(f + h * 64 + sub * 8))[0] = a0;
+    ((float4*)(f + h * 64 + sub * 8))[1] = a1;
+    const float4 z0 = ((const float4*)(O + 88 + sub * 8))[0], z1 = ((const float4*)(O + 88 + sub * 8))[1];
+    ((float4*)(f + 768 + h * 64 + sub * 8))[0] = z0;
+    ((float4*)(f + 768 + h * 64 + sub * 8))[1] = z1;
+  }
   const float* R = rotb + (size_t)bl * 9;
   const float txx = trans[bl * 3 + 0], tyy = trans[bl * 3 + 1], tzz = trans[bl * 3 + 2];
-#pragma unroll
-  for (int p = 0; p < 8; p++) {
-    const float dx = O[64 + p * 3 + 0] - txx;
-    const float dy = O[64 + p * 3 + 1] - tyy;
-    const float dz = O[64 + p * 3 + 2] - tzz;
+  {
+    const float dx = O[64 + sub * 3 + 0] - txx;
+    const float dy = O[64 + sub * 3 + 1] - tyy;
+    const float dz = O[64 + sub * 3 + 2] - tzz;
     const float lx = R[0] * dx + R[3] * dy + R[6] * dz;
     const float ly = R[1] * dx + R[4] * dy + R[7] * dz;
     const float lz = R[2] * dx + R[5] * dy + R[8] * dz;
-    f[512 + h * 24 + p * 3 + 0] = lx;
-    f[512 + h * 24 + p * 3 + 1] = ly;
-    f[512 + h * 24 + p * 3 + 2] = lz;
-    f[704 + h * 8 + p] = sqrtf(lx * lx + ly * ly + lz * lz + 1e-8f);
-  }
-  for (int c = 0; c < 64; c++) f[768 + h * 64 + c] = O[88 + c];
+    f[512 + h * 24 + sub * 3 + 0] = lx;
+    f[512 + h * 24 + sub * 3 + 1] = ly;
+    f[512 + h * 24 + sub * 3 + 2] = lz;
+    f[704 + h * 8 + sub] = sqrtf(lx * lx + ly * ly + lz * lz + 1e-8f);
+  }
 }
 
 __global__ __launch_bounds__(64) void ln_k(const float* __restrict__ x, const float* __restrict__ resid,
@@ -634,23 +661,46 @@
   }
 }
 
-__global__ __launch_bounds__(64) void final_k(const float* __restrict__ sF, const float* __restrict__ sipa,
-                                              const float* __restrict__ rotb, const float* __restrict__ trans,
-                                              const float* __restrict__ hpost, const float* __restrict__ rowsum,
-                                              const float* __restrict__ Wbb, const float* __restrict__ bbb,
-                                              const int* __restrict__ flagp, void* __restrict__ outv) {
+__global__ __launch_bounds__(64) void lnfinal_k(const float* __restrict__ x , const float* __restrict__ resid ,
+                                                const float* __restrict__ g, const float* __restrict__ bta,
+                                                const float* __restrict__ sF, const float* __restrict__ rotb,
+                                                const float* __restrict__ trans, const float* __restrict__ hpost,
+                                                const float* __restrict__ rowsum, const float* __restrict__ Wbb,
+                                                const float* __restrict__ bbb, const int* __restrict__ flagp,
+                                                void* __restrict__ outv) {
   const int bl = blockIdx.x, t = threadIdx.x;
   const int flag = flagp[0];
   bf16* outb = (bf16*)outv;
   float* outf = (float*)outv;
-  const float* si = sipa + (size_t)bl * CSD;
-  float d6[6] = {0.f, 0.f, 0.f, 0.f, 0.f, 0.f};
+  const float* xr = x + (size_t)bl * CSD;
+  const float* rr = resid + (size_t)bl * CSD;
+  float v[6];
+  float s = 0.f;
 #pragma unroll
   for (int e = 0; e < 6; e++) {
     const int c = t + e * 64;
-    const float v = si[c];
-#pragma unroll
-    for (int u = 0; u < 6; u++) d6[u] = fmaf(v, Wbb[c * 6 + u], d6[u]);
+    v[e] = xr[c] + rr[c];
+    s += v[e];
+  }
+  s = wredf(s);
+  const float mu = s * (1.f / 384.f);
+  float var = 0.f;
+#pragma unroll
+  for (int e = 0; e < 6; e++) { const float d = v[e] - mu; var = fmaf(d, d, var); }
+  var = wredf(var) * (1.f / 384.f);
+  const float inv = rsqrtf(var + 1e-5f);
+  float si6[6];
+#pragma unroll
+  for (int e = 0; e < 6; e++) {
+    const int c = t + e * 64;
+    si6[e] = (v[e] - mu) * inv * g[c] + bta[c];
+  }
+  float d6[6] = {0.f, 0.f, 0.f, 0.f, 0.f, 0.f};
+#pragma unroll
+  for (int e = 0; e < 6; e++) {
+    const int c = t + e * 64;
+#pragma unroll
+    for (int u = 0; u < 6; u++) d6[u] = fmaf(si6[e], Wbb[c * 6 + u], d6[u]);
   }
 #pragma unroll
   for (int u = 0; u < 6; u++) d6[u] = wredf(d6[u]);
@@ -659,12 +709,12 @@
   for (int u = 0; u < 6; u++) upd[u] = d6[u] + bbb[u];
   const float* R = rotb + (size_t)bl * 9;
   if (t == 0) {
-    float w = 1.f, x = upd[0], y = upd[1], z = upd[2];
-    const float iq = rsqrtf(w * w + x * x + y * y + z * z + 1e-8f);
-    w *= iq; x *= iq; y *= iq; z *= iq;
-    const float Ru[9] = {1.f - 2.f * (y * y + z * z), 2.f * (x * y - w * z), 2.f * (x * z + w * y),
-                         2.f * (x * y + w * z), 1.f - 2.f * (x * x + z * z), 2.f * (y * z - w * x),
-                         2.f * (x * z - w * y), 2.f * (y * z + w * x), 1.f - 2.f * (x * x + y * y)};
+    float w = 1.f, x2 = upd[0], y = upd[1], z = upd[2];
+    const float iq = rsqrtf(w * w + x2 * x2 + y * y + z * z + 1e-8f);
+    w *= iq; x2 *= iq; y *= iq; z *= iq;
+    const float Ru[9] = {1.f - 2.f * (y * y + z * z), 2.f * (x2 * y - w * z), 2.f * (x2 * z + w * y),
+                         2.f * (x2 * y + w * z), 1.f - 2.f * (x2 * x2 + z * z), 2.f * (y * z - w * x2),
+                         2.f * (x2 * z - w * y), 2.f * (y * z + w * x2), 1.f - 2.f * (x2 * x2 + y * y)};
 #pragma unroll
     for (int i = 0; i < 3; i++)
 #pragma unroll
@@ -686,7 +736,7 @@
 #pragma unroll
   for (int e = 0; e < 6; e++) {
     const int c = t + e * 64;
-    const float sv = sr[c], sp = si[c];
+    const float sv = sr[c], sp = si6[e];
     const size_t base = (size_t)bl * 4 * CSD + c;
     const float o0 = rs0 * sv + hp0 * sp;
     const float o1 = rs1 * sv + hp1 * sp;
@@ -730,39 +780,30 @@
   short* Qb     = (short*)(ws + WS_QB);
   short* Kb     = (short*)(ws + WS_KB);
   short* Vtb    = (short*)(ws + WS_VT);
-  short* Vrow   = (short*)(ws + WS_VROW);
   float* Oext   = ws + WS_PROJ;
   float* featb  = ws + WS_QB;
   float* x1s1   = ws + WS_PROJ;
-  float* t1b    = ws + WS_QB;
-  float* t2b    = ws + WS_KB;
-  float* x3     = ws + WS_PROJ + 1572864;
-  float* sipa   = ws + WS_KB;
+  float* t1b    = ws + WS_PROJ + 1572864;
+  float* t2b    = ws + WS_PROJ + 3145728;
+  float* x3     = ws + WS_PROJ + 4718592;
 
   detect_k<<<1, 64, 0, stream>>>((const unsigned int*)d_in[5], flag);
   cvtall_k<<<(IN_END + 255) / 256, 256, 0, stream>>>(ptrs, ws, flag);
-  wcatT_k<<<2880, 256, 0, stream>>>(ws + OFF_WQ, ws + OFF_WK, ws + OFF_WV,
-                                    ws + OFF_WQP, ws + OFF_WKP, ws + OFF_WVP, WcatT);
-  wT_k<<<1920, 256, 0, stream>>>(ws + OFF_WO, WoT, FEATD, CSD);
-  wT_k<<<576, 256, 0, stream>>>(ws + OFF_WT1, Wt1T, CSD, CSD);
-  wT_k<<<576, 256, 0, stream>>>(ws + OFF_WT2, Wt2T, CSD, CSD);
-  wT_k<<<576, 256, 0, stream>>>(ws + OFF_WT3, Wt3T, CSD, CSD);
+  wprep_k<<<1632, 256, 0, stream>>>(ws, (short*)ws);
   wreduce_k<<<24, 256, 0, stream>>>(ws + OFF_WPOST, ws + OFF_WRES, WpostR, WresR);
   mhc_k<<<BL, 64, 0, stream>>>(sF, ws + OFF_QUAT, ws + OFF_BPOST, ws + OFF_BRES, ws + OFF_ALPHA,
                                WpostR, WresR, hpost, rowsum, rotb);
   gemm_mfma_k<<<dim3(15, 32), 256, 0, stream>>>(sF, WcatT, nullptr, proj, BL, NPROJ, CSD, 0);
-  assemble_k<<<128, 256, 0, stream>>>(proj, rotb, ws + OFF_TRANS, ws + OFF_Z1, ws + OFF_Z2,
-                                      ws + OFF_WZQ, ws + OFF_WZK, ws + OFF_HEADW,
-                                      (int*)Qb, (int*)Kb, (int*)Vrow);
-  vtrans_k<<<dim3(16, 32), 256, 0, stream>>>(Vrow, Vtb);
+  assemble_k<<<BL, 64, 0, stream>>>(proj, rotb, ws + OFF_TRANS, d_in[1], d_in[2],
+                                    ws + OFF_WZQ, ws + OFF_WZK, ws + OFF_HEADW, flag, Qb, Kb, Vtb);
   attn_k<<<512, 512, 0, stream>>>(Qb, Kb, Vtb, ws + OFF_MASK, Oext);
-  feat_k<<<128, 256, 0, stream>>>(Oext, rotb, ws + OFF_TRANS, featb);
+  feat_k<<<BL, 64, 0, stream>>>(Oext, rotb, ws + OFF_TRANS, featb);
   gemm_mfma_k<<<dim3(3, 32), 256, 0, stream>>>(featb, WoT, ws + OFF_BO, x1s1, BL, CSD, FEATD, 0);
   ln_k<<<BL, 64, 0, stream>>>(x1s1, sF, ws + OFF_LN1G, ws + OFF_LN1B, x1s1);
   gemm_mfma_k<<<dim3(3, 32), 256, 0, stream>>>(x1s1, Wt1T, ws + OFF_BT1, t1b, BL, CSD, CSD, 1);
   gemm_mfma_k<<<dim3(3, 32), 256, 0, stream>>>(t1b, Wt2T, ws + OFF_BT2, t2b, BL, CSD, CSD, 1);
   gemm_mfma_k<<<dim3(3, 32), 256, 0, stream>>>(t2b, Wt3T, ws + OFF_BT3, x3, BL, CSD, CSD, 0);
-  ln_k<<<BL, 64, 0, stream>>>(x3, x1s1, ws + OFF_LNTG, ws + OFF_LNTB, sipa);
-  final_k<<<BL, 64, 0, stream>>>(sF, sipa, rotb, ws + OFF_TRANS, hpost, rowsum,
-                                 ws + OFF_WBB, ws + OFF_BBB, flag, d_out);
-}
+  lnfinal_k<<<BL, 64, 0, stream>>>(x3, x1s1, ws + OFF_LNTG, ws + OFF_LNTB, sF, rotb,
+                                   ws + OFF_TRANS, hpost, rowsum, ws + OFF_WBB, ws + OFF_BBB,
+                                   flag, d_out);
+}
```

Measured after the change: 584.5 us. 7.7% more time.
